# Performance work log

Hardware: AMD Instinct MI355X
Metric: run time of the kernel (lower is better)

The kernel has to match this reference:

```python
import jax, jax.numpy as jnp
import numpy as np

IN_FEATURES = 8192
OUT_FEATURES = 8192
CODESZ = 8            # E8 lattice dimension per code index
CODEBOOK_SIZE = 65536 # 2^16-entry codebook (16-bit indices)
TOKENS = 32           # decode-style batch


def fwht(x):
    """Fast Walsh-Hadamard transform (Sylvester order) along the last axis.
    n must be a power of 2. Unnormalized (multiply by H_n)."""
    n = x.shape[-1]
    steps = int(np.log2(n))
    h = 1
    for _ in range(steps):
        y = x.reshape(*x.shape[:-1], n // (2 * h), 2, h)
        a = y[..., 0, :]
        b = y[..., 1, :]
        x = jnp.stack([a + b, a - b], axis=-2).reshape(*y.shape[:-3], n)
        h *= 2
    return x


def setup_inputs() -> dict:
    key = jax.random.key(0)
    k0, k1, k2, k3, k4 = jax.random.split(key, 5)
    x = jax.random.normal(k0, (TOKENS, IN_FEATURES), dtype=jnp.float32)
    # learned codebook: CODEBOOK_SIZE vectors of CODESZ entries (E8P-like lattice points)
    codebook_table = jax.random.normal(k1, (CODEBOOK_SIZE, CODESZ), dtype=jnp.float32) * 0.1
    # quantized weight indices: [out_features, in_features // codesz]
    Qidxs = jax.random.randint(k2, (OUT_FEATURES, IN_FEATURES // CODESZ), 0, CODEBOOK_SIZE, dtype=jnp.int32)
    # random sign vectors (incoherence processing)
    SU = (2.0 * jax.random.randint(k3, (IN_FEATURES,), 0, 2) - 1.0).astype(jnp.float32)
    SV = (2.0 * jax.random.randint(k4, (OUT_FEATURES,), 0, 2) - 1.0).astype(jnp.float32)
    Wscale = jnp.array(0.02, dtype=jnp.float32)
    return {"x": x, "codebook_table": codebook_table, "Qidxs": Qidxs,
            "SU": SU, "SV": SV, "Wscale": Wscale}


def reference(x, codebook_table, Qidxs, SU, SV, Wscale):
    n_in = x.shape[-1]
    n_out = SV.shape[0]
    # input incoherence: sign flip then orthonormal Hadamard rotation (matmul_hadUt)
    xh = fwht(x * SU) * (1.0 / jnp.sqrt(jnp.float32(n_in)))  # [T, n_in]
    # codebook dequantization: gather lattice vectors and lay out as [n_out, n_in]
    W = codebook_table[Qidxs].reshape(n_out, n_in)
    # quantized matmul in the rotated basis
    z = xh @ W.T  # [T, n_out]
    # output rotation (matmul_hadU) + sign/scale (SV absorbs Wscale in the torch code)
    out = fwht(z) * (1.0 / jnp.sqrt(jnp.float32(n_out))) * (SV * Wscale)
    return out
```

## Files before the change

### kernel.cpp

```cpp
#include <hip/hip_runtime.h>
#include <hip/hip_bf16.h>


typedef __attribute__((ext_vector_type(16))) float f32x16;
typedef __attribute__((ext_vector_type(8))) __bf16 bf16x8;
typedef __attribute__((ext_vector_type(4))) __bf16 bf16x4;
typedef __attribute__((ext_vector_type(4))) int i32x4;

#define IN_F 8192
#define OUT_F 8192
#define TOKENS 32
#define KSPLIT 8
#define KCHUNK 1024
#define CH (KCHUNK / 8)
#define GROUPS (KCHUNK / 32)
#define DG 5
#define DI 7
#define INV_SQRT_8192 0.011048543456039806f
#define PAD(i) ((i) + ((i) >> 5))

#if __has_builtin(__builtin_amdgcn_raw_buffer_load_b128) && \
    __has_builtin(__builtin_amdgcn_make_buffer_rsrc)
#define HAVE_BUF 1
#else
#define HAVE_BUF 0
#endif

__device__ inline void fwht8_reg(float* v) {
    #pragma unroll
    for (int h = 1; h < 8; h <<= 1)
        #pragma unroll
        for (int i = 0; i < 8; i += 2 * h)
            #pragma unroll
            for (int j = 0; j < h; ++j) {
                float a = v[i + j], b = v[i + j + h];
                v[i + j] = a + b;
                v[i + j + h] = a - b;
            }
}

__device__ inline void fwht1024(float v[4], float* st, int tid) {
    {
        float t0 = v[0] + v[1], t1 = v[0] - v[1];
        float t2 = v[2] + v[3], t3 = v[2] - v[3];
        v[0] = t0 + t2; v[1] = t1 + t3; v[2] = t0 - t2; v[3] = t1 - t3;
    }
    int pos[4] = {4 * tid, 4 * tid + 1, 4 * tid + 2, 4 * tid + 3};
    #pragma unroll
    for (int s = 1; s < 5; ++s) {
        #pragma unroll
        for (int j = 0; j < 4; ++j) st[PAD(pos[j])] = v[j];
        __syncthreads();
        const int q = 1 << (2 * s);
        const int i = ((tid >> (2 * s)) << (2 * s + 2)) + (tid & (q - 1));
        #pragma unroll
        for (int j = 0; j < 4; ++j) { pos[j] = i + j * q; v[j] = st[PAD(pos[j])]; }
        __syncthreads();
        float t0 = v[0] + v[1], t1 = v[0] - v[1];
        float t2 = v[2] + v[3], t3 = v[2] - v[3];
        v[0] = t0 + t2; v[1] = t1 + t3; v[2] = t0 - t2; v[3] = t1 - t3;
    }
}

__global__ __launch_bounds__(256)
void prepA_kernel(const float* __restrict__ x, const float* __restrict__ su,
                  float* __restrict__ xw) {
    const int id = blockIdx.x * 256 + threadIdx.x;
    const int t = id >> 10, c = id & 1023;
    float v[8];
    #pragma unroll
    for (int k = 0; k < 8; ++k)
        v[k] = x[t * IN_F + k * 1024 + c] * su[k * 1024 + c];
    fwht8_reg(v);
    #pragma unroll
    for (int k = 0; k < 8; ++k)
        xw[t * IN_F + k * 1024 + c] = v[k];
}

__global__ __launch_bounds__(256)
void prepB_kernel(const float* __restrict__ cb, __bf16* __restrict__ cbb,
                  const float* __restrict__ xw, __bf16* __restrict__ xh) {
    __shared__ float st[1056];
    const int tid = threadIdx.x;
    if (blockIdx.x < 512) {
        int i = blockIdx.x * 256 + tid;
        float4 vv = ((const float4*)cb)[i];
        bf16x4 o;
        o[0] = (__bf16)vv.x; o[1] = (__bf16)vv.y;
        o[2] = (__bf16)vv.z; o[3] = (__bf16)vv.w;
        ((bf16x4*)cbb)[i] = o;
        return;
    }
    const int id = blockIdx.x - 512;
    const int t = id >> 3, ch = id & 7;
    const float* src = xw + (size_t)t * IN_F + ch * 1024;
    float4 f = ((const float4*)src)[tid];
    float v[4] = {f.x, f.y, f.z, f.w};
    fwht1024(v, st, tid);
    __bf16* dst = xh + (size_t)t * IN_F + ch * 1024;
    #pragma unroll
    for (int j = 0; j < 4; ++j)
        dst[tid + j * 256] = (__bf16)(v[j] * INV_SQRT_8192);
}

__global__ __launch_bounds__(512, 4)
void qgemm_kernel(const int* __restrict__ qidxs,
                  const __bf16* __restrict__ cb,
                  const __bf16* __restrict__ xh,
                  __bf16* __restrict__ zpart) {
    __shared__ __align__(16) __bf16 xt[TOKENS * KCHUNK];
    const int ks = blockIdx.x & (KSPLIT - 1);
    const int nb = blockIdx.x >> 3;
    const int tid = threadIdx.x;
    const int wave = tid >> 6, lane = tid & 63;
    const int h = lane >> 5, lc = lane & 31;
    const int n = nb * 256 + wave * 32 + lc;

    #pragma unroll
    for (int i = 0; i < 8; ++i) {
        int f = i * 512 + tid, r = f >> 7, c = f & 127;
        i32x4 v = *(const i32x4*)(xh + (size_t)r * IN_F + ks * KCHUNK + c * 8);
        *(i32x4*)(xt + ((r * CH + (c ^ (r & 7))) << 3)) = v;
    }
    __syncthreads();

    const int* qrow = qidxs + (size_t)n * (IN_F / 8) + ks * (KCHUNK / 8);

#if HAVE_BUF
    __amdgpu_buffer_rsrc_t rsrc = __builtin_amdgcn_make_buffer_rsrc(
        (void*)cb, (short)0, 65536 * 16, 0x00020000);
    #define GA(ix, au) __builtin_bit_cast(bf16x8, \
        __builtin_amdgcn_raw_buffer_load_b128(rsrc, (ix) << 4, 0, au))
#else
    const bf16x8* cbv = (const bf16x8*)cb;
    #define GA(ix, au) (cbv[ix])
#endif

    f32x16 acc;
    #pragma unroll
    for (int i = 0; i < 16; ++i) acc[i] = 0.f;

    i32x4 iv[GROUPS];
    bf16x8 bfr[GROUPS][2];

    #pragma unroll
    for (int g = 0; g < DI; ++g)
        iv[g] = *(const i32x4*)(qrow + g * 4);
    #pragma unroll
    for (int g = 0; g < DG; ++g) {
        if (g & 1) {
            bfr[g][0] = GA(h ? iv[g][1] : iv[g][0], 1);
            bfr[g][1] = GA(h ? iv[g][3] : iv[g][2], 1);
        } else {
            bfr[g][0] = GA(h ? iv[g][1] : iv[g][0], 0);
            bfr[g][1] = GA(h ? iv[g][3] : iv[g][2], 0);
        }
    }

    #pragma unroll
    for (int g = 0; g < GROUPS; ++g) {
        if (g + DI < GROUPS)
            iv[g + DI] = *(const i32x4*)(qrow + (g + DI) * 4);
        if (g + DG < GROUPS) {
            if ((g + DG) & 1) {
                bfr[g + DG][0] = GA(h ? iv[g + DG][1] : iv[g + DG][0], 1);
                bfr[g + DG][1] = GA(h ? iv[g + DG][3] : iv[g + DG][2], 1);
            } else {
                bfr[g + DG][0] = GA(h ? iv[g + DG][1] : iv[g + DG][0], 0);
                bfr[g + DG][1] = GA(h ? iv[g + DG][3] : iv[g + DG][2], 0);
            }
        }
        #pragma unroll
        for (int sgi = 0; sgi < 2; ++sgi) {
            const int T = 2 * g + sgi;
            bf16x8 a = *(const bf16x8*)(xt +
                          ((lc * CH + ((2 * T + h) ^ (lc & 7))) << 3));
            acc = __builtin_amdgcn_mfma_f32_32x32x16_bf16(a, bfr[g][sgi],
                                                          acc, 0, 0, 0);
        }
    }

    __bf16* zp = zpart + ((size_t)ks * TOKENS) * OUT_F + n;
    #pragma unroll
    for (int r = 0; r < 16; ++r) {
        int m = (r & 3) + 4 * h + 8 * (r >> 2);
        zp[(size_t)m * OUT_F] = (__bf16)acc[r];
    }
}

__global__ __launch_bounds__(256)
void zsumA_kernel(const __bf16* __restrict__ zpart, float* __restrict__ z1) {
    __shared__ float st[1056];
    const int tid = threadIdx.x;
    const int t = blockIdx.x >> 3, ch = blockIdx.x & 7;
    float v[4] = {0.f, 0.f, 0.f, 0.f};
    #pragma unroll
    for (int ks = 0; ks < KSPLIT; ++ks) {
        bf16x4 b = *(const bf16x4*)(zpart +
                     ((size_t)(ks * TOKENS + t)) * OUT_F + ch * 1024 + tid * 4);
        v[0] += (float)b[0]; v[1] += (float)b[1];
        v[2] += (float)b[2]; v[3] += (float)b[3];
    }
    fwht1024(v, st, tid);
    float* dst = z1 + (size_t)t * OUT_F + ch * 1024;
    #pragma unroll
    for (int j = 0; j < 4; ++j)
        dst[tid + j * 256] = v[j];
}

__global__ __launch_bounds__(256)
void zsumB_kernel(const float* __restrict__ z1, const float* __restrict__ sv,
                  const float* __restrict__ wscale, float* __restrict__ out) {
    const int id = blockIdx.x * 256 + threadIdx.x;
    const int t = id >> 10, c = id & 1023;
    float v[8];
    #pragma unroll
    for (int k = 0; k < 8; ++k)
        v[k] = z1[t * OUT_F + k * 1024 + c];
    fwht8_reg(v);
    const float sc = INV_SQRT_8192 * wscale[0];
    #pragma unroll
    for (int k = 0; k < 8; ++k)
        out[t * OUT_F + k * 1024 + c] = v[k] * sc * sv[k * 1024 + c];
}

extern "C" void kernel_launch(void* const* d_in, const int* in_sizes, int n_in,
                              void* d_out, int out_size, void* d_ws, size_t ws_size,
                              hipStream_t stream) {
    const float* x      = (const float*)d_in[0];
    const float* cb     = (const float*)d_in[1];
    const int*   qidxs  = (const int*)d_in[2];
    const float* su     = (const float*)d_in[3];
    const float* sv     = (const float*)d_in[4];
    const float* wscale = (const float*)d_in[5];
    float* out = (float*)d_out;

    char* ws = (char*)d_ws;
    __bf16* cb_bf16 = (__bf16*)ws;
    __bf16* xh      = (__bf16*)(ws + (1u << 20));
    __bf16* zpart   = (__bf16*)(ws + (1u << 20) + (512u << 10));
    float*  xw      = (float*)(ws + (5u << 20) + (512u << 10));
    float*  z1      = (float*)(ws + (6u << 20) + (512u << 10));

    hipLaunchKernelGGL(prepA_kernel, dim3(128), dim3(256), 0, stream,
                       x, su, xw);
    hipLaunchKernelGGL(prepB_kernel, dim3(768), dim3(256), 0, stream,
                       cb, cb_bf16, xw, xh);
    hipLaunchKernelGGL(qgemm_kernel, dim3(32 * KSPLIT), dim3(512), 0, stream,
                       qidxs, cb_bf16, xh, zpart);
    hipLaunchKernelGGL(zsumA_kernel, dim3(256), dim3(256), 0, stream,
                       zpart, z1);
    hipLaunchKernelGGL(zsumB_kernel, dim3(128), dim3(256), 0, stream,
                       z1, sv, wscale, out);
}
```

Measured before the change: 127.8 us.

## Fuse 8-point Hadamard stage into prep and zsum kernels, dropping two launches

The separate 8-point Walsh-Hadamard kernels (prepA, zsumB) are removed. Each 1024-chunk block now computes its own row of the 8x8 Hadamard stage directly, as a signed sum over all 8 chunks. This cuts two kernel launches and the fp32 intermediate buffers xw and z1. In exchange, each block reads 8x more input: x and su in prep, and all 8 chunks of every zpart split in zsum, so redundant global reads go up.

```diff
diff --git a/kernel.cpp b/kernel.cpp
--- a/kernel.cpp
+++ b/kernel.cpp
@@ -26,19 +26,6 @@
 #define HAVE_BUF 0
 #endif
 
-__device__ inline void fwht8_reg(float* v) {
-    #pragma unroll
-    for (int h = 1; h < 8; h <<= 1)
-        #pragma unroll
-        for (int i = 0; i < 8; i += 2 * h)
-            #pragma unroll
-            for (int j = 0; j < h; ++j) {
-                float a = v[i + j], b = v[i + j + h];
-                v[i + j] = a + b;
-                v[i + j + h] = a - b;
-            }
-}
-
 __device__ inline void fwht1024(float v[4], float* st, int tid) {
     {
         float t0 = v[0] + v[1], t1 = v[0] - v[1];
@@ -63,23 +50,9 @@
 }
 
 __global__ __launch_bounds__(256)
-void prepA_kernel(const float* __restrict__ x, const float* __restrict__ su,
-                  float* __restrict__ xw) {
-    const int id = blockIdx.x * 256 + threadIdx.x;
-    const int t = id >> 10, c = id & 1023;
-    float v[8];
-    #pragma unroll
-    for (int k = 0; k < 8; ++k)
-        v[k] = x[t * IN_F + k * 1024 + c] * su[k * 1024 + c];
-    fwht8_reg(v);
-    #pragma unroll
-    for (int k = 0; k < 8; ++k)
-        xw[t * IN_F + k * 1024 + c] = v[k];
-}
-
-__global__ __launch_bounds__(256)
-void prepB_kernel(const float* __restrict__ cb, __bf16* __restrict__ cbb,
-                  const float* __restrict__ xw, __bf16* __restrict__ xh) {
+void prep_kernel(const float* __restrict__ cb, __bf16* __restrict__ cbb,
+                 const float* __restrict__ x, const float* __restrict__ su,
+                 __bf16* __restrict__ xh) {
     __shared__ float st[1056];
     const int tid = threadIdx.x;
     if (blockIdx.x < 512) {
@@ -93,9 +66,20 @@
     }
     const int id = blockIdx.x - 512;
     const int t = id >> 3, ch = id & 7;
-    const float* src = xw + (size_t)t * IN_F + ch * 1024;
-    float4 f = ((const float4*)src)[tid];
-    float v[4] = {f.x, f.y, f.z, f.w};
+    float sgn[8];
+    #pragma unroll
+    for (int k = 0; k < 8; ++k)
+        sgn[k] = (__builtin_popcount(ch & k) & 1) ? -1.f : 1.f;
+    float v[4] = {0.f, 0.f, 0.f, 0.f};
+    #pragma unroll
+    for (int k = 0; k < 8; ++k) {
+        float4 xv = *(const float4*)(x + (size_t)t * IN_F + k * 1024 + tid * 4);
+        float4 sv4 = *(const float4*)(su + k * 1024 + tid * 4);
+        v[0] += sgn[k] * xv.x * sv4.x;
+        v[1] += sgn[k] * xv.y * sv4.y;
+        v[2] += sgn[k] * xv.z * sv4.z;
+        v[3] += sgn[k] * xv.w * sv4.w;
+    }
     fwht1024(v, st, tid);
     __bf16* dst = xh + (size_t)t * IN_F + ch * 1024;
     #pragma unroll
@@ -189,39 +173,42 @@
 }
 
 __global__ __launch_bounds__(256)
-void zsumA_kernel(const __bf16* __restrict__ zpart, float* __restrict__ z1) {
+void zsum_kernel(const __bf16* __restrict__ zpart, const float* __restrict__ sv,
+                 const float* __restrict__ wscale, float* __restrict__ out) {
     __shared__ float st[1056];
     const int tid = threadIdx.x;
     const int t = blockIdx.x >> 3, ch = blockIdx.x & 7;
+    float sgn[8];
+    #pragma unroll
+    for (int k = 0; k < 8; ++k)
+        sgn[k] = (__builtin_popcount(ch & k) & 1) ? -1.f : 1.f;
+    float a0[8] = {0,0,0,0,0,0,0,0}, a1[8] = {0,0,0,0,0,0,0,0};
+    float a2[8] = {0,0,0,0,0,0,0,0}, a3[8] = {0,0,0,0,0,0,0,0};
+    #pragma unroll
+    for (int ks = 0; ks < KSPLIT; ++ks) {
+        const __bf16* zr = zpart + ((size_t)(ks * TOKENS + t)) * OUT_F + tid * 4;
+        #pragma unroll
+        for (int kk = 0; kk < 8; ++kk) {
+            bf16x4 b = *(const bf16x4*)(zr + kk * 1024);
+            a0[kk] += (float)b[0]; a1[kk] += (float)b[1];
+            a2[kk] += (float)b[2]; a3[kk] += (float)b[3];
+        }
+    }
     float v[4] = {0.f, 0.f, 0.f, 0.f};
     #pragma unroll
-    for (int ks = 0; ks < KSPLIT; ++ks) {
-        bf16x4 b = *(const bf16x4*)(zpart +
-                     ((size_t)(ks * TOKENS + t)) * OUT_F + ch * 1024 + tid * 4);
-        v[0] += (float)b[0]; v[1] += (float)b[1];
-        v[2] += (float)b[2]; v[3] += (float)b[3];
+    for (int kk = 0; kk < 8; ++kk) {
+        v[0] += sgn[kk] * a0[kk];
+        v[1] += sgn[kk] * a1[kk];
+        v[2] += sgn[kk] * a2[kk];
+        v[3] += sgn[kk] * a3[kk];
     }
     fwht1024(v, st, tid);
-    float* dst = z1 + (size_t)t * OUT_F + ch * 1024;
+    const float sc = INV_SQRT_8192 * wscale[0];
+    float* dst = out + (size_t)t * OUT_F + ch * 1024;
+    const float* svp = sv + ch * 1024;
     #pragma unroll
     for (int j = 0; j < 4; ++j)
-        dst[tid + j * 256] = v[j];
-}
-
-__global__ __launch_bounds__(256)
-void zsumB_kernel(const float* __restrict__ z1, const float* __restrict__ sv,
-                  const float* __restrict__ wscale, float* __restrict__ out) {
-    const int id = blockIdx.x * 256 + threadIdx.x;
-    const int t = id >> 10, c = id & 1023;
-    float v[8];
-    #pragma unroll
-    for (int k = 0; k < 8; ++k)
-        v[k] = z1[t * OUT_F + k * 1024 + c];
-    fwht8_reg(v);
-    const float sc = INV_SQRT_8192 * wscale[0];
-    #pragma unroll
-    for (int k = 0; k < 8; ++k)
-        out[t * OUT_F + k * 1024 + c] = v[k] * sc * sv[k * 1024 + c];
+        dst[tid + j * 256] = v[j] * sc * svp[tid + j * 256];
 }
 
 extern "C" void kernel_launch(void* const* d_in, const int* in_sizes, int n_in,
@@ -239,17 +226,11 @@
     __bf16* cb_bf16 = (__bf16*)ws;
     __bf16* xh      = (__bf16*)(ws + (1u << 20));
     __bf16* zpart   = (__bf16*)(ws + (1u << 20) + (512u << 10));
-    float*  xw      = (float*)(ws + (5u << 20) + (512u << 10));
-    float*  z1      = (float*)(ws + (6u << 20) + (512u << 10));
-
-    hipLaunchKernelGGL(prepA_kernel, dim3(128), dim3(256), 0, stream,
-                       x, su, xw);
-    hipLaunchKernelGGL(prepB_kernel, dim3(768), dim3(256), 0, stream,
-                       cb, cb_bf16, xw, xh);
+
+    hipLaunchKernelGGL(prep_kernel, dim3(768), dim3(256), 0, stream,
+                       cb, cb_bf16, x, su, xh);
     hipLaunchKernelGGL(qgemm_kernel, dim3(32 * KSPLIT), dim3(512), 0, stream,
                        qidxs, cb_bf16, xh, zpart);
-    hipLaunchKernelGGL(zsumA_kernel, dim3(256), dim3(256), 0, stream,
-                       zpart, z1);
-    hipLaunchKernelGGL(zsumB_kernel, dim3(128), dim3(256), 0, stream,
-                       z1, sv, wscale, out);
-}
+    hipLaunchKernelGGL(zsum_kernel, dim3(256), dim3(256), 0, stream,
+                       zpart, sv, wscale, out);
+}
```

Result: slower. 132.1 us (+3.4%).

## Fuse five pipeline kernels into one cooperative kernel with grid syncs

Applied to the files above, without the earlier changes.

Merges the prep, Hadamard, quantized GEMM and output-transform stages into a single cooperative launch of 256 blocks, separated by grid-wide barriers. Each stage body is factored into device functions, and work is remapped onto 512-thread blocks, with two 256-thread FWHT groups per block and half-block tasks for the elementwise stages. This removes the per-kernel launch gaps between the five stages. In exchange it pays for four grid syncs and threadfences, and launch bounds of (512,2) may change register allocation for the GEMM stage. A fallback to the old multi-kernel path remains when cooperative launch is unsupported.

```diff
diff --git a/kernel.cpp b/kernel.cpp
--- a/kernel.cpp
+++ b/kernel.cpp
@@ -1,5 +1,8 @@
 #include <hip/hip_runtime.h>
 #include <hip/hip_bf16.h>
+#include <hip/hip_cooperative_groups.h>
+
+namespace cg = cooperative_groups;
 
 
 typedef __attribute__((ext_vector_type(16))) float f32x16;
@@ -62,11 +65,19 @@
     }
 }
 
-__global__ __launch_bounds__(256)
-void prepA_kernel(const float* __restrict__ x, const float* __restrict__ su,
-                  float* __restrict__ xw) {
-    const int id = blockIdx.x * 256 + threadIdx.x;
-    const int t = id >> 10, c = id & 1023;
+__device__ inline void cvt_body(const float* __restrict__ cb,
+                                __bf16* __restrict__ cbb, int g) {
+    float4 vv = ((const float4*)cb)[g];
+    bf16x4 o;
+    o[0] = (__bf16)vv.x; o[1] = (__bf16)vv.y;
+    o[2] = (__bf16)vv.z; o[3] = (__bf16)vv.w;
+    ((bf16x4*)cbb)[g] = o;
+}
+
+__device__ inline void prepA_body(const float* __restrict__ x,
+                                  const float* __restrict__ su,
+                                  float* __restrict__ xw, int task) {
+    const int t = task >> 10, c = task & 1023;
     float v[8];
     #pragma unroll
     for (int k = 0; k < 8; ++k)
@@ -77,41 +88,61 @@
         xw[t * IN_F + k * 1024 + c] = v[k];
 }
 
-__global__ __launch_bounds__(256)
-void prepB_kernel(const float* __restrict__ cb, __bf16* __restrict__ cbb,
-                  const float* __restrict__ xw, __bf16* __restrict__ xh) {
-    __shared__ float st[1056];
-    const int tid = threadIdx.x;
-    if (blockIdx.x < 512) {
-        int i = blockIdx.x * 256 + tid;
-        float4 vv = ((const float4*)cb)[i];
-        bf16x4 o;
-        o[0] = (__bf16)vv.x; o[1] = (__bf16)vv.y;
-        o[2] = (__bf16)vv.z; o[3] = (__bf16)vv.w;
-        ((bf16x4*)cbb)[i] = o;
-        return;
-    }
-    const int id = blockIdx.x - 512;
+__device__ inline void prepB_body(const float* __restrict__ xw,
+                                  __bf16* __restrict__ xh,
+                                  float* st, int id, int tl) {
     const int t = id >> 3, ch = id & 7;
-    const float* src = xw + (size_t)t * IN_F + ch * 1024;
-    float4 f = ((const float4*)src)[tid];
+    float4 f = ((const float4*)(xw + (size_t)t * IN_F + ch * 1024))[tl];
     float v[4] = {f.x, f.y, f.z, f.w};
-    fwht1024(v, st, tid);
+    fwht1024(v, st, tl);
     __bf16* dst = xh + (size_t)t * IN_F + ch * 1024;
     #pragma unroll
     for (int j = 0; j < 4; ++j)
-        dst[tid + j * 256] = (__bf16)(v[j] * INV_SQRT_8192);
-}
-
-__global__ __launch_bounds__(512, 4)
-void qgemm_kernel(const int* __restrict__ qidxs,
-                  const __bf16* __restrict__ cb,
-                  const __bf16* __restrict__ xh,
-                  __bf16* __restrict__ zpart) {
-    __shared__ __align__(16) __bf16 xt[TOKENS * KCHUNK];
-    const int ks = blockIdx.x & (KSPLIT - 1);
-    const int nb = blockIdx.x >> 3;
-    const int tid = threadIdx.x;
+        dst[tl + j * 256] = (__bf16)(v[j] * INV_SQRT_8192);
+}
+
+__device__ inline void zsumA_body(const __bf16* __restrict__ zpart,
+                                  float* __restrict__ z1,
+                                  float* st, int id, int tl) {
+    const int t = id >> 3, ch = id & 7;
+    float v[4] = {0.f, 0.f, 0.f, 0.f};
+    #pragma unroll
+    for (int ks = 0; ks < KSPLIT; ++ks) {
+        bf16x4 b = *(const bf16x4*)(zpart +
+                     ((size_t)(ks * TOKENS + t)) * OUT_F + ch * 1024 + tl * 4);
+        v[0] += (float)b[0]; v[1] += (float)b[1];
+        v[2] += (float)b[2]; v[3] += (float)b[3];
+    }
+    fwht1024(v, st, tl);
+    float* dst = z1 + (size_t)t * OUT_F + ch * 1024;
+    #pragma unroll
+    for (int j = 0; j < 4; ++j)
+        dst[tl + j * 256] = v[j];
+}
+
+__device__ inline void zsumB_body(const float* __restrict__ z1,
+                                  const float* __restrict__ sv,
+                                  const float* __restrict__ wscale,
+                                  float* __restrict__ out, int task) {
+    const int t = task >> 10, c = task & 1023;
+    float v[8];
+    #pragma unroll
+    for (int k = 0; k < 8; ++k)
+        v[k] = z1[t * OUT_F + k * 1024 + c];
+    fwht8_reg(v);
+    const float sc = INV_SQRT_8192 * wscale[0];
+    #pragma unroll
+    for (int k = 0; k < 8; ++k)
+        out[t * OUT_F + k * 1024 + c] = v[k] * sc * sv[k * 1024 + c];
+}
+
+__device__ inline void qgemm_body(const int* __restrict__ qidxs,
+                                  const __bf16* __restrict__ cb,
+                                  const __bf16* __restrict__ xh,
+                                  __bf16* __restrict__ zpart,
+                                  __bf16* xt, int bid, int tid) {
+    const int ks = bid & (KSPLIT - 1);
+    const int nb = bid >> 3;
     const int wave = tid >> 6, lane = tid & 63;
     const int h = lane >> 5, lc = lane & 31;
     const int n = nb * 256 + wave * 32 + lc;
@@ -179,6 +210,7 @@
                                                           acc, 0, 0, 0);
         }
     }
+    #undef GA
 
     __bf16* zp = zpart + ((size_t)ks * TOKENS) * OUT_F + n;
     #pragma unroll
@@ -188,40 +220,82 @@
     }
 }
 
+__global__ __launch_bounds__(512, 2)
+void fused_kernel(const float* __restrict__ x, const float* __restrict__ cb,
+                  const int* __restrict__ qidxs, const float* __restrict__ su,
+                  const float* __restrict__ sv,
+                  const float* __restrict__ wscale, float* __restrict__ out,
+                  __bf16* __restrict__ cbb, __bf16* __restrict__ xh,
+                  __bf16* __restrict__ zpart, float* __restrict__ xw,
+                  float* __restrict__ z1) {
+    cg::grid_group grid = cg::this_grid();
+    __shared__ __align__(16) char smem[65536];
+    float* smf = (float*)smem;
+    const int tid = threadIdx.x;
+    const int bid = blockIdx.x;
+
+    cvt_body(cb, cbb, bid * 512 + tid);
+    if (tid < 128)
+        prepA_body(x, su, xw, bid * 128 + tid);
+    __threadfence();
+    grid.sync();
+
+    if (bid < 128)
+        prepB_body(xw, xh, smf + (tid >> 8) * 1056,
+                   bid * 2 + (tid >> 8), tid & 255);
+    __threadfence();
+    grid.sync();
+
+    qgemm_body(qidxs, cbb, xh, zpart, (__bf16*)smem, bid, tid);
+    __threadfence();
+    grid.sync();
+
+    if (bid < 128)
+        zsumA_body(zpart, z1, smf + (tid >> 8) * 1056,
+                   bid * 2 + (tid >> 8), tid & 255);
+    __threadfence();
+    grid.sync();
+
+    if (tid < 128)
+        zsumB_body(z1, sv, wscale, out, bid * 128 + tid);
+}
+
+__global__ __launch_bounds__(256)
+void prepA_kernel(const float* __restrict__ x, const float* __restrict__ su,
+                  float* __restrict__ xw) {
+    prepA_body(x, su, xw, blockIdx.x * 256 + threadIdx.x);
+}
+
+__global__ __launch_bounds__(256)
+void prepB_kernel(const float* __restrict__ cb, __bf16* __restrict__ cbb,
+                  const float* __restrict__ xw, __bf16* __restrict__ xh) {
+    __shared__ float st[1056];
+    if (blockIdx.x < 512) {
+        cvt_body(cb, cbb, blockIdx.x * 256 + threadIdx.x);
+        return;
+    }
+    prepB_body(xw, xh, st, blockIdx.x - 512, threadIdx.x);
+}
+
+__global__ __launch_bounds__(512, 4)
+void qgemm_kernel(const int* __restrict__ qidxs,
+                  const __bf16* __restrict__ cb,
+                  const __bf16* __restrict__ xh,
+                  __bf16* __restrict__ zpart) {
+    __shared__ __align__(16) __bf16 xt[TOKENS * KCHUNK];
+    qgemm_body(qidxs, cb, xh, zpart, xt, blockIdx.x, threadIdx.x);
+}
+
 __global__ __launch_bounds__(256)
 void zsumA_kernel(const __bf16* __restrict__ zpart, float* __restrict__ z1) {
     __shared__ float st[1056];
-    const int tid = threadIdx.x;
-    const int t = blockIdx.x >> 3, ch = blockIdx.x & 7;
-    float v[4] = {0.f, 0.f, 0.f, 0.f};
-    #pragma unroll
-    for (int ks = 0; ks < KSPLIT; ++ks) {
-        bf16x4 b = *(const bf16x4*)(zpart +
-                     ((size_t)(ks * TOKENS + t)) * OUT_F + ch * 1024 + tid * 4);
-        v[0] += (float)b[0]; v[1] += (float)b[1];
-        v[2] += (float)b[2]; v[3] += (float)b[3];
-    }
-    fwht1024(v, st, tid);
-    float* dst = z1 + (size_t)t * OUT_F + ch * 1024;
-    #pragma unroll
-    for (int j = 0; j < 4; ++j)
-        dst[tid + j * 256] = v[j];
+    zsumA_body(zpart, z1, st, blockIdx.x, threadIdx.x);
 }
 
 __global__ __launch_bounds__(256)
 void zsumB_kernel(const float* __restrict__ z1, const float* __restrict__ sv,
                   const float* __restrict__ wscale, float* __restrict__ out) {
-    const int id = blockIdx.x * 256 + threadIdx.x;
-    const int t = id >> 10, c = id & 1023;
-    float v[8];
-    #pragma unroll
-    for (int k = 0; k < 8; ++k)
-        v[k] = z1[t * OUT_F + k * 1024 + c];
-    fwht8_reg(v);
-    const float sc = INV_SQRT_8192 * wscale[0];
-    #pragma unroll
-    for (int k = 0; k < 8; ++k)
-        out[t * OUT_F + k * 1024 + c] = v[k] * sc * sv[k * 1024 + c];
+    zsumB_body(z1, sv, wscale, out, blockIdx.x * 256 + threadIdx.x);
 }
 
 extern "C" void kernel_launch(void* const* d_in, const int* in_sizes, int n_in,
@@ -236,20 +310,38 @@
     float* out = (float*)d_out;
 
     char* ws = (char*)d_ws;
-    __bf16* cb_bf16 = (__bf16*)ws;
-    __bf16* xh      = (__bf16*)(ws + (1u << 20));
-    __bf16* zpart   = (__bf16*)(ws + (1u << 20) + (512u << 10));
-    float*  xw      = (float*)(ws + (5u << 20) + (512u << 10));
-    float*  z1      = (float*)(ws + (6u << 20) + (512u << 10));
-
-    hipLaunchKernelGGL(prepA_kernel, dim3(128), dim3(256), 0, stream,
-                       x, su, xw);
-    hipLaunchKernelGGL(prepB_kernel, dim3(768), dim3(256), 0, stream,
-                       cb, cb_bf16, xw, xh);
-    hipLaunchKernelGGL(qgemm_kernel, dim3(32 * KSPLIT), dim3(512), 0, stream,
-                       qidxs, cb_bf16, xh, zpart);
-    hipLaunchKernelGGL(zsumA_kernel, dim3(256), dim3(256), 0, stream,
-                       zpart, z1);
-    hipLaunchKernelGGL(zsumB_kernel, dim3(128), dim3(256), 0, stream,
-                       z1, sv, wscale, out);
-}
+    __bf16* cbb   = (__bf16*)ws;
+    __bf16* xh    = (__bf16*)(ws + (1u << 20));
+    __bf16* zpart = (__bf16*)(ws + (1u << 20) + (512u << 10));
+    float*  xw    = (float*)(ws + (5u << 20) + (512u << 10));
+    float*  z1    = (float*)(ws + (6u << 20) + (512u << 10));
+
+    static int coop = -1;
+    if (coop < 0) {
+        int dev = 0;
+        hipGetDevice(&dev);
+        hipDeviceProp_t p{};
+        hipGetDeviceProperties(&p, dev);
+        coop = p.cooperativeLaunch ? 1 : 0;
+    }
+
+    if (coop) {
+        void* kargs[] = { (void*)&x, (void*)&cb, (void*)&qidxs, (void*)&su,
+                          (void*)&sv, (void*)&wscale, (void*)&out,
+                          (void*)&cbb, (void*)&xh, (void*)&zpart,
+                          (void*)&xw, (void*)&z1 };
+        hipLaunchCooperativeKernel((const void*)fused_kernel, dim3(256),
+                                   dim3(512), kargs, 0, stream);
+    } else {
+        hipLaunchKernelGGL(prepA_kernel, dim3(128), dim3(256), 0, stream,
+                           x, su, xw);
+        hipLaunchKernelGGL(prepB_kernel, dim3(768), dim3(256), 0, stream,
+                           cb, cbb, xw, xh);
+        hipLaunchKernelGGL(qgemm_kernel, dim3(32 * KSPLIT), dim3(512), 0,
+                           stream, qidxs, cbb, xh, zpart);
+        hipLaunchKernelGGL(zsumA_kernel, dim3(256), dim3(256), 0, stream,
+                           zpart, z1);
+        hipLaunchKernelGGL(zsumB_kernel, dim3(128), dim3(256), 0, stream,
+                           z1, sv, wscale, out);
+    }
+}
```

Result: slower. 426.8 us (+234.0%).

## Fuse input sign/H8 stage into prep kernel and use wave shuffles in FWHT1024

Applied to the files above, without the earlier changes.

Removes the separate prepA launch and its xw round trip: each prep block now rebuilds its 1024-chunk of the 8-point Hadamard stage directly from x and SU using precomputed signs, at the cost of every chunk block rereading all eight chunks of x. The 1024-point FWHT now runs its first 64-wide butterflies with cross-lane shuffles, followed by a single shared-memory transpose and a final radix-4 stage. This replaces four shared-memory exchanges and eight barriers with one exchange. The change also applies to the output FWHT used in zsumA.

```diff
diff --git a/kernel.cpp b/kernel.cpp
--- a/kernel.cpp
+++ b/kernel.cpp
@@ -26,60 +26,35 @@
 #define HAVE_BUF 0
 #endif
 
-__device__ inline void fwht8_reg(float* v) {
-    #pragma unroll
-    for (int h = 1; h < 8; h <<= 1)
+__device__ inline void h4_reg(float v[4]) {
+    float t0 = v[0] + v[1], t1 = v[0] - v[1];
+    float t2 = v[2] + v[3], t3 = v[2] - v[3];
+    v[0] = t0 + t2; v[1] = t1 + t3; v[2] = t0 - t2; v[3] = t1 - t3;
+}
+
+__device__ inline void fwht1024(float v[4], float* st, int tid) {
+    h4_reg(v);
+    const int lane = tid & 63;
+    #pragma unroll
+    for (int m = 1; m < 64; m <<= 1) {
         #pragma unroll
-        for (int i = 0; i < 8; i += 2 * h)
-            #pragma unroll
-            for (int j = 0; j < h; ++j) {
-                float a = v[i + j], b = v[i + j + h];
-                v[i + j] = a + b;
-                v[i + j + h] = a - b;
-            }
-}
-
-__device__ inline void fwht1024(float v[4], float* st, int tid) {
-    {
-        float t0 = v[0] + v[1], t1 = v[0] - v[1];
-        float t2 = v[2] + v[3], t3 = v[2] - v[3];
-        v[0] = t0 + t2; v[1] = t1 + t3; v[2] = t0 - t2; v[3] = t1 - t3;
-    }
-    int pos[4] = {4 * tid, 4 * tid + 1, 4 * tid + 2, 4 * tid + 3};
-    #pragma unroll
-    for (int s = 1; s < 5; ++s) {
-        #pragma unroll
-        for (int j = 0; j < 4; ++j) st[PAD(pos[j])] = v[j];
-        __syncthreads();
-        const int q = 1 << (2 * s);
-        const int i = ((tid >> (2 * s)) << (2 * s + 2)) + (tid & (q - 1));
-        #pragma unroll
-        for (int j = 0; j < 4; ++j) { pos[j] = i + j * q; v[j] = st[PAD(pos[j])]; }
-        __syncthreads();
-        float t0 = v[0] + v[1], t1 = v[0] - v[1];
-        float t2 = v[2] + v[3], t3 = v[2] - v[3];
-        v[0] = t0 + t2; v[1] = t1 + t3; v[2] = t0 - t2; v[3] = t1 - t3;
-    }
+        for (int j = 0; j < 4; ++j) {
+            float p = __shfl_xor(v[j], m, 64);
+            v[j] = (lane & m) ? (p - v[j]) : (v[j] + p);
+        }
+    }
+    #pragma unroll
+    for (int j = 0; j < 4; ++j) st[PAD(4 * tid + j)] = v[j];
+    __syncthreads();
+    #pragma unroll
+    for (int j = 0; j < 4; ++j) v[j] = st[PAD(tid + j * 256)];
+    h4_reg(v);
 }
 
 __global__ __launch_bounds__(256)
-void prepA_kernel(const float* __restrict__ x, const float* __restrict__ su,
-                  float* __restrict__ xw) {
-    const int id = blockIdx.x * 256 + threadIdx.x;
-    const int t = id >> 10, c = id & 1023;
-    float v[8];
-    #pragma unroll
-    for (int k = 0; k < 8; ++k)
-        v[k] = x[t * IN_F + k * 1024 + c] * su[k * 1024 + c];
-    fwht8_reg(v);
-    #pragma unroll
-    for (int k = 0; k < 8; ++k)
-        xw[t * IN_F + k * 1024 + c] = v[k];
-}
-
-__global__ __launch_bounds__(256)
-void prepB_kernel(const float* __restrict__ cb, __bf16* __restrict__ cbb,
-                  const float* __restrict__ xw, __bf16* __restrict__ xh) {
+void prep_kernel(const float* __restrict__ cb, __bf16* __restrict__ cbb,
+                 const float* __restrict__ x, const float* __restrict__ su,
+                 __bf16* __restrict__ xh) {
     __shared__ float st[1056];
     const int tid = threadIdx.x;
     if (blockIdx.x < 512) {
@@ -93,9 +68,20 @@
     }
     const int id = blockIdx.x - 512;
     const int t = id >> 3, ch = id & 7;
-    const float* src = xw + (size_t)t * IN_F + ch * 1024;
-    float4 f = ((const float4*)src)[tid];
-    float v[4] = {f.x, f.y, f.z, f.w};
+    float sgn[8];
+    #pragma unroll
+    for (int k = 0; k < 8; ++k)
+        sgn[k] = (__builtin_popcount(ch & k) & 1) ? -1.f : 1.f;
+    float v[4] = {0.f, 0.f, 0.f, 0.f};
+    #pragma unroll
+    for (int k = 0; k < 8; ++k) {
+        float4 xv = *(const float4*)(x + (size_t)t * IN_F + k * 1024 + tid * 4);
+        float4 s4 = *(const float4*)(su + k * 1024 + tid * 4);
+        v[0] += sgn[k] * xv.x * s4.x;
+        v[1] += sgn[k] * xv.y * s4.y;
+        v[2] += sgn[k] * xv.z * s4.z;
+        v[3] += sgn[k] * xv.w * s4.w;
+    }
     fwht1024(v, st, tid);
     __bf16* dst = xh + (size_t)t * IN_F + ch * 1024;
     #pragma unroll
@@ -217,7 +203,16 @@
     #pragma unroll
     for (int k = 0; k < 8; ++k)
         v[k] = z1[t * OUT_F + k * 1024 + c];
-    fwht8_reg(v);
+    #pragma unroll
+    for (int h = 1; h < 8; h <<= 1)
+        #pragma unroll
+        for (int i = 0; i < 8; i += 2 * h)
+            #pragma unroll
+            for (int j = 0; j < h; ++j) {
+                float a = v[i + j], b = v[i + j + h];
+                v[i + j] = a + b;
+                v[i + j + h] = a - b;
+            }
     const float sc = INV_SQRT_8192 * wscale[0];
     #pragma unroll
     for (int k = 0; k < 8; ++k)
@@ -236,18 +231,15 @@
     float* out = (float*)d_out;
 
     char* ws = (char*)d_ws;
-    __bf16* cb_bf16 = (__bf16*)ws;
-    __bf16* xh      = (__bf16*)(ws + (1u << 20));
-    __bf16* zpart   = (__bf16*)(ws + (1u << 20) + (512u << 10));
-    float*  xw      = (float*)(ws + (5u << 20) + (512u << 10));
-    float*  z1      = (float*)(ws + (6u << 20) + (512u << 10));
-
-    hipLaunchKernelGGL(prepA_kernel, dim3(128), dim3(256), 0, stream,
-                       x, su, xw);
-    hipLaunchKernelGGL(prepB_kernel, dim3(768), dim3(256), 0, stream,
-                       cb, cb_bf16, xw, xh);
+    __bf16* cbb   = (__bf16*)ws;
+    __bf16* xh    = (__bf16*)(ws + (1u << 20));
+    __bf16* zpart = (__bf16*)(ws + (1u << 20) + (512u << 10));
+    float*  z1    = (float*)(ws + (5u << 20) + (512u << 10));
+
+    hipLaunchKernelGGL(prep_kernel, dim3(768), dim3(256), 0, stream,
+                       cb, cbb, x, su, xh);
     hipLaunchKernelGGL(qgemm_kernel, dim3(32 * KSPLIT), dim3(512), 0, stream,
-                       qidxs, cb_bf16, xh, zpart);
+                       qidxs, cbb, xh, zpart);
     hipLaunchKernelGGL(zsumA_kernel, dim3(256), dim3(256), 0, stream,
                        zpart, z1);
     hipLaunchKernelGGL(zsumB_kernel, dim3(128), dim3(256), 0, stream,
```

Result: no change. 127.8 us (-0.0%).
